# Optimization experiments

Hardware: AMD Instinct MI355X
Metric: run time of the kernel (lower is better)

## Reference

```python
import jax, jax.numpy as jnp
import numpy as np

EPS = 1e-5
DECAY = 0.9        # membrane potential decay
SLOPE = 0.01       # leaky_relu negative slope
HEBB_LR = 0.01     # Hebbian plasticity learning rate
WD = 1e-3          # synapse weight decay
W_CLAMP = 1.0      # synapse weight clamp


def _ln(x, g, b):
    mu = jnp.mean(x, axis=-1, keepdims=True)
    var = jnp.mean((x - mu) ** 2, axis=-1, keepdims=True)
    return (x - mu) * jax.lax.rsqrt(var + EPS) * g + b


def setup_inputs() -> dict:
    key = jax.random.key(0)
    ks = jax.random.split(key, 4)
    B, N = 16384, 1024
    scale = 1.0 / np.sqrt(N)
    return {
        "inputs": jax.random.normal(ks[0], (B, N), dtype=jnp.float32),
        "contribution": jax.random.uniform(ks[1], (B,), dtype=jnp.float32),
        "prev_potential": jnp.zeros((B, N), dtype=jnp.float32),
        "syn_weights": jax.random.normal(ks[2], (N, N), dtype=jnp.float32) * scale,
        "gate_W": jax.random.normal(ks[3], (N, N), dtype=jnp.float32) * scale,
        "gate_b": jnp.zeros((N,), dtype=jnp.float32),
        "pre_gamma": jnp.ones((N,), dtype=jnp.float32),
        "pre_beta": jnp.zeros((N,), dtype=jnp.float32),
        "ln_gamma": jnp.ones((N,), dtype=jnp.float32),
        "ln_beta": jnp.zeros((N,), dtype=jnp.float32),
    }


def reference(inputs, contribution, prev_potential, syn_weights, gate_W, gate_b,
              pre_gamma, pre_beta, ln_gamma, ln_beta):
    B = inputs.shape[0]
    # pre-norm
    x_norm = _ln(inputs, pre_gamma, pre_beta)
    # neuron: recurrent drive through synapse weights + leaky membrane
    pre = x_norm @ syn_weights                      # [B, N]
    potential = DECAY * prev_potential + pre        # new neuron state
    activation = jnp.where(potential >= 0, potential, SLOPE * potential)
    # Hebbian synapse update modulated by per-sample contribution
    hebb = jnp.einsum('bi,bj->ij', activation * contribution[:, None], activation) / B
    new_syn_weights = jnp.clip(syn_weights * (1.0 - WD) + HEBB_LR * hebb,
                               -W_CLAMP, W_CLAMP)
    # gated residual (gate computed on raw inputs)
    gate = jax.nn.sigmoid(inputs @ gate_W.T + gate_b)
    residual = gate * activation + (1.0 - gate) * inputs
    # post-norm (dropout is identity in eval/reference)
    output = _ln(residual, ln_gamma, ln_beta)
    return (output, potential, new_syn_weights)
```

## Files before the change

### kernel.cpp

```cpp
#include <hip/hip_runtime.h>
#include <cstdint>
#include <cstddef>

#define EPS 1e-5f
#define DECAY 0.9f
#define SLOPE 0.01f
#define HEBB_LR 0.01f
#define WDK 1e-3f

typedef float f32x4 __attribute__((ext_vector_type(4)));
typedef __bf16 bf16x8 __attribute__((ext_vector_type(8)));
typedef unsigned short u16;
typedef unsigned int u32;

union U128 { uint4 u; bf16x8 b; };
union Pack16 { u16 s[16]; uint4 q[2]; };
union Pack8  { u16 s[8];  uint4 q; };
union Pack4  { u16 s[4];  uint2 q; };

__device__ __forceinline__ u16 f2b(float f) {
  u32 u = __builtin_bit_cast(u32, f);
  u = u + 0x7FFFu + ((u >> 16) & 1u);
  return (u16)(u >> 16);
}
__device__ __forceinline__ float b2f(u16 h) {
  u32 u = ((u32)h) << 16;
  return __builtin_bit_cast(float, u);
}
__device__ __forceinline__ float wred(float x) {
#pragma unroll
  for (int o = 32; o > 0; o >>= 1) x += __shfl_down(x, o, 64);
  return x;
}

__device__ __forceinline__ void gld16(const u16* g, u16* lds) {
  __builtin_amdgcn_global_load_lds(
      (__attribute__((address_space(1))) void*)g,
      (__attribute__((address_space(3))) void*)lds, 16, 0, 0);
}

__global__ __launch_bounds__(256) void prep_rows(
    const float* __restrict__ in, const float* __restrict__ pg,
    const float* __restrict__ pb, u16* __restrict__ xnb,
    u16* __restrict__ inb, int N) {
  const int row = blockIdx.x, t = threadIdx.x;
  const float* rp = in + (size_t)row * N;
  float4 v = reinterpret_cast<const float4*>(rp)[t];
  float s = v.x + v.y + v.z + v.w;
  float s2 = v.x * v.x + v.y * v.y + v.z * v.z + v.w * v.w;
  s = wred(s); s2 = wred(s2);
  __shared__ float rs_[4], rs2_[4];
  if ((t & 63) == 0) { rs_[t >> 6] = s; rs2_[t >> 6] = s2; }
  __syncthreads();
  float S = rs_[0] + rs_[1] + rs_[2] + rs_[3];
  float S2 = rs2_[0] + rs2_[1] + rs2_[2] + rs2_[3];
  float mu = S / N;
  float var = S2 / N - mu * mu;
  float rstd = rsqrtf(var + EPS);
  float4 g = reinterpret_cast<const float4*>(pg)[t];
  float4 b = reinterpret_cast<const float4*>(pb)[t];
  float xv[4] = {v.x, v.y, v.z, v.w};
  float gv[4] = {g.x, g.y, g.z, g.w};
  float bv[4] = {b.x, b.y, b.z, b.w};
  Pack4 px, pi;
#pragma unroll
  for (int j = 0; j < 4; ++j) {
    px.s[j] = f2b((xv[j] - mu) * rstd * gv[j] + bv[j]);
    pi.s[j] = f2b(xv[j]);
  }
  reinterpret_cast<uint2*>(xnb + (size_t)row * N)[t] = px.q;
  reinterpret_cast<uint2*>(inb + (size_t)row * N)[t] = pi.q;
}

__global__ __launch_bounds__(256) void wconv(const float* __restrict__ W,
                                             u16* __restrict__ Wb, int total) {
  int idx = blockIdx.x * 256 + threadIdx.x;
  size_t off = (size_t)idx * 8;
  if (off >= (size_t)total) return;
  float4 a = *reinterpret_cast<const float4*>(W + off);
  float4 b = *reinterpret_cast<const float4*>(W + off + 4);
  Pack8 p;
  p.s[0] = f2b(a.x); p.s[1] = f2b(a.y); p.s[2] = f2b(a.z); p.s[3] = f2b(a.w);
  p.s[4] = f2b(b.x); p.s[5] = f2b(b.y); p.s[6] = f2b(b.z); p.s[7] = f2b(b.w);
  *reinterpret_cast<uint4*>(Wb + off) = p.q;
}

__global__ __launch_bounds__(256) void wconv_T(const float* __restrict__ W,
                                               u16* __restrict__ Wt, int R, int C) {
  __shared__ float tile[64][65];
  int c0 = blockIdx.x * 64, r0 = blockIdx.y * 64;
  int tr = threadIdx.x >> 2, tc = threadIdx.x & 3;
#pragma unroll
  for (int cc = 0; cc < 4; ++cc) {
    float4 v = *reinterpret_cast<const float4*>(W + (size_t)(r0 + tr) * C + c0 + tc * 16 + cc * 4);
    tile[tr][tc * 16 + cc * 4 + 0] = v.x;
    tile[tr][tc * 16 + cc * 4 + 1] = v.y;
    tile[tr][tc * 16 + cc * 4 + 2] = v.z;
    tile[tr][tc * 16 + cc * 4 + 3] = v.w;
  }
  __syncthreads();
  Pack16 p;
#pragma unroll
  for (int j = 0; j < 16; ++j) p.s[j] = f2b(tile[tc * 16 + j][tr]);
  uint4* dst = reinterpret_cast<uint4*>(Wt + (size_t)(c0 + tr) * R + r0 + tc * 16);
  dst[0] = p.q[0]; dst[1] = p.q[1];
}

__global__ __launch_bounds__(256) void transpose_act(
    const float* __restrict__ pot, const float* __restrict__ contrib,
    u16* __restrict__ actT, u16* __restrict__ actcT, int Brows, int N) {
  __shared__ float tile[64][65];
  __shared__ float csh[64];
  int n0 = blockIdx.x * 64, b0 = blockIdx.y * 64;
  int tr = threadIdx.x >> 2, tc = threadIdx.x & 3;
  if (threadIdx.x < 64) csh[threadIdx.x] = contrib[b0 + threadIdx.x];
#pragma unroll
  for (int cc = 0; cc < 4; ++cc) {
    float4 v = *reinterpret_cast<const float4*>(pot + (size_t)(b0 + tr) * N + n0 + tc * 16 + cc * 4);
    float a0 = v.x >= 0.f ? v.x : SLOPE * v.x;
    float a1 = v.y >= 0.f ? v.y : SLOPE * v.y;
    float a2 = v.z >= 0.f ? v.z : SLOPE * v.z;
    float a3 = v.w >= 0.f ? v.w : SLOPE * v.w;
    tile[tr][tc * 16 + cc * 4 + 0] = a0;
    tile[tr][tc * 16 + cc * 4 + 1] = a1;
    tile[tr][tc * 16 + cc * 4 + 2] = a2;
    tile[tr][tc * 16 + cc * 4 + 3] = a3;
  }
  __syncthreads();
  Pack16 pa, pc;
#pragma unroll
  for (int j = 0; j < 16; ++j) {
    float a = tile[tc * 16 + j][tr];
    pa.s[j] = f2b(a);
    pc.s[j] = f2b(a * csh[tc * 16 + j]);
  }
  size_t obase = (size_t)(n0 + tr) * Brows + b0 + tc * 16;
  uint4* d1 = reinterpret_cast<uint4*>(actT + obase);
  d1[0] = pa.q[0]; d1[1] = pa.q[1];
  uint4* d2 = reinterpret_cast<uint4*>(actcT + obase);
  d2[0] = pc.q[0]; d2[1] = pc.q[1];
}

__global__ __launch_bounds__(256) void fuse_out(
    const float* __restrict__ pot, const u16* __restrict__ gate,
    const float* __restrict__ in, const float* __restrict__ lg,
    const float* __restrict__ lb, float* __restrict__ out, int N) {
  const int row = blockIdx.x, t = threadIdx.x;
  size_t base = (size_t)row * N;
  float4 p = reinterpret_cast<const float4*>(pot + base)[t];
  float4 x = reinterpret_cast<const float4*>(in + base)[t];
  Pack4 gq; gq.q = reinterpret_cast<const uint2*>(gate + base)[t];
  float pv[4] = {p.x, p.y, p.z, p.w}, xv[4] = {x.x, x.y, x.z, x.w};
  float res[4];
  float s = 0.f, s2 = 0.f;
#pragma unroll
  for (int j = 0; j < 4; ++j) {
    float a = pv[j] >= 0.f ? pv[j] : SLOPE * pv[j];
    float gv = b2f(gq.s[j]);
    float r = gv * a + (1.f - gv) * xv[j];
    res[j] = r; s += r; s2 += r * r;
  }
  s = wred(s); s2 = wred(s2);
  __shared__ float rs_[4], rs2_[4];
  if ((t & 63) == 0) { rs_[t >> 6] = s; rs2_[t >> 6] = s2; }
  __syncthreads();
  float S = rs_[0] + rs_[1] + rs_[2] + rs_[3];
  float S2 = rs2_[0] + rs2_[1] + rs2_[2] + rs2_[3];
  float mu = S / N, var = S2 / N - mu * mu, rstd = rsqrtf(var + EPS);
  float4 g4 = reinterpret_cast<const float4*>(lg)[t];
  float4 b4 = reinterpret_cast<const float4*>(lb)[t];
  float gv[4] = {g4.x, g4.y, g4.z, g4.w}, bv[4] = {b4.x, b4.y, b4.z, b4.w};
  float4 o;
  o.x = (res[0] - mu) * rstd * gv[0] + bv[0];
  o.y = (res[1] - mu) * rstd * gv[1] + bv[1];
  o.z = (res[2] - mu) * rstd * gv[2] + bv[2];
  o.w = (res[3] - mu) * rstd * gv[3] + bv[3];
  reinterpret_cast<float4*>(out + base)[t] = o;
}

__device__ __forceinline__ u32 swz64(u32 b) { return b ^ (((b >> 7) & 3u) << 4); }

__device__ __forceinline__ void stage8(int s, int NT4, const u16* A, const u16* Bt,
                                       int m0, int n0, int lda, int kbase,
                                       char* ldsc, int tid) {
  if (s >= NT4) return;
  const int tau = s >> 2, j = s & 3;
  const int mat = j & 1, ks = j >> 1;
  const u16* src = mat ? Bt : A;
  const int rbase = mat ? n0 : m0;
  const int kk = kbase + tau * 64 + ks * 32;
  char* dst = ldsc + (tau & 1) * 65536 + mat * 32768 + ks * 16384 + tid * 16;
  const int row = tid >> 2;
  const int kg = (tid & 3) ^ ((tid >> 3) & 3);
  const u16* g0 = src + (size_t)(rbase + row) * (size_t)lda + kk + kg * 8;
  gld16(g0, (u16*)dst);
  gld16(g0 + (size_t)128 * (size_t)lda, (u16*)(dst + 8192));
}

#define VMW(n) asm volatile("s_waitcnt vmcnt(" #n ")" ::: "memory")
#define BARR() asm volatile("s_barrier" ::: "memory")

template <int EPI>
__global__ __launch_bounds__(512, 2) void gemm8p(
    const u16* __restrict__ A, const u16* __restrict__ Bt,
    int lda, int NT, int Ncols,
    const float* __restrict__ aux,
    float* __restrict__ outF, u16* __restrict__ outB,
    int nbx, int nbxShift, int nbyX) {
  __shared__ __align__(128) u16 lds[65536];
  char* ldsc = (char*)lds;
  const int tid = threadIdx.x;
  const int w = tid >> 6, l = tid & 63;
  const int wr = w >> 2, wc = w & 3;
  const int r16 = l & 15, gq = l >> 4;

  int bx, by, kb;
  if (EPI == 2) {
    bx = blockIdx.x; by = blockIdx.y; kb = blockIdx.z * NT * 64;
  } else {
    int bid = blockIdx.x;
    int xcd = bid & 7, i = bid >> 3;
    by = xcd * nbyX + (i >> nbxShift);
    bx = i & (nbx - 1);
    kb = 0;
  }
  const int m0 = by * 256, n0 = bx * 256;
  const int NT4 = NT * 4;

  int pA[8], pB[4];
#pragma unroll
  for (int mf = 0; mf < 8; ++mf)
    pA[mf] = (int)swz64((u32)((wr * 128 + mf * 16 + r16) * 64 + gq * 16));
#pragma unroll
  for (int nf = 0; nf < 4; ++nf)
    pB[nf] = (int)swz64((u32)((wc * 64 + nf * 16 + r16) * 64 + gq * 16));

  f32x4 acc[8][4] = {};
  U128 af[8], bf[2];

#define LDA_(ks) { char* _b = ldsc + buf * 65536 + (ks) * 16384;              \
  _Pragma("unroll") for (int mf = 0; mf < 8; ++mf)                            \
    af[mf].u = *reinterpret_cast<const uint4*>(_b + pA[mf]); }
#define LDB_(ks, nh) { char* _b = ldsc + buf * 65536 + 32768 + (ks) * 16384;  \
  bf[0].u = *reinterpret_cast<const uint4*>(_b + pB[2 * (nh)]);               \
  bf[1].u = *reinterpret_cast<const uint4*>(_b + pB[2 * (nh) + 1]); }
#define MFMA_(nh) { __builtin_amdgcn_s_setprio(1);                            \
  _Pragma("unroll") for (int mf = 0; mf < 8; ++mf) {                          \
    acc[mf][2 * (nh)] = __builtin_amdgcn_mfma_f32_16x16x32_bf16(              \
        af[mf].b, bf[0].b, acc[mf][2 * (nh)], 0, 0, 0);                       \
    acc[mf][2 * (nh) + 1] = __builtin_amdgcn_mfma_f32_16x16x32_bf16(          \
        af[mf].b, bf[1].b, acc[mf][2 * (nh) + 1], 0, 0, 0); }                 \
  __builtin_amdgcn_s_setprio(0); }
#define STG(s) stage8((s), NT4, A, Bt, m0, n0, lda, kb, ldsc, tid)

  for (int s = 0; s < 6; ++s) STG(s);
  VMW(8); BARR();

  for (int t = 0; t < NT - 1; ++t) {
    const int buf = t & 1;
    const int sb = t * 4;
    LDA_(0); LDB_(0, 0); STG(sb + 6); VMW(8); BARR(); MFMA_(0); BARR();
    LDB_(0, 1);          STG(sb + 7); VMW(8); BARR(); MFMA_(1); BARR();
    LDA_(1); LDB_(1, 0); STG(sb + 8); VMW(8); BARR(); MFMA_(0); BARR();
    LDB_(1, 1);          STG(sb + 9);
    if (t == NT - 2) { VMW(4); } else { VMW(8); }
    BARR(); MFMA_(1); BARR();
  }
  {
    const int buf = (NT - 1) & 1;
    LDA_(0); LDB_(0, 0); MFMA_(0);
    LDB_(0, 1);          MFMA_(1);
    VMW(0); BARR();
    LDA_(1); LDB_(1, 0); MFMA_(0);
    LDB_(1, 1);          MFMA_(1);
  }
#undef LDA_
#undef LDB_
#undef MFMA_
#undef STG

  const size_t splitOff =
      (EPI == 2) ? (size_t)blockIdx.z * (size_t)Ncols * (size_t)(gridDim.y * 256) : 0;
#pragma unroll
  for (int mf = 0; mf < 8; ++mf) {
#pragma unroll
    for (int r = 0; r < 4; ++r) {
      const int m = m0 + wr * 128 + mf * 16 + gq * 4 + r;
#pragma unroll
      for (int nf = 0; nf < 4; ++nf) {
        const int n = n0 + wc * 64 + nf * 16 + r16;
        float v = acc[mf][nf][r];
        if (EPI == 0) {
          size_t off = (size_t)m * Ncols + n;
          outF[off] = DECAY * aux[off] + v;
        } else if (EPI == 1) {
          float gl = v + aux[n];
          outB[(size_t)m * Ncols + n] = f2b(1.f / (1.f + __expf(-gl)));
        } else {
          outB[splitOff + (size_t)m * Ncols + n] = f2b(v);
        }
      }
    }
  }
}

__global__ __launch_bounds__(256) void syn_update(
    const float* __restrict__ syn, const u16* __restrict__ part,
    float* __restrict__ outS, int total8, float hebbScale, int nsplit, int NN) {
  int idx = blockIdx.x * 256 + threadIdx.x;
  if (idx >= total8) return;
  float h[8] = {0.f, 0.f, 0.f, 0.f, 0.f, 0.f, 0.f, 0.f};
  for (int sp = 0; sp < nsplit; ++sp) {
    Pack8 p;
    p.q = reinterpret_cast<const uint4*>(part + (size_t)sp * NN)[idx];
#pragma unroll
    for (int j = 0; j < 8; ++j) h[j] += b2f(p.s[j]);
  }
  float4 s0 = reinterpret_cast<const float4*>(syn)[idx * 2];
  float4 s1 = reinterpret_cast<const float4*>(syn)[idx * 2 + 1];
  float sv[8] = {s0.x, s0.y, s0.z, s0.w, s1.x, s1.y, s1.z, s1.w};
  float ov[8];
#pragma unroll
  for (int j = 0; j < 8; ++j)
    ov[j] = fminf(1.f, fmaxf(-1.f, sv[j] * (1.f - WDK) + hebbScale * h[j]));
  float4 o0 = {ov[0], ov[1], ov[2], ov[3]};
  float4 o1 = {ov[4], ov[5], ov[6], ov[7]};
  reinterpret_cast<float4*>(outS)[idx * 2] = o0;
  reinterpret_cast<float4*>(outS)[idx * 2 + 1] = o1;
}

extern "C" void kernel_launch(void* const* d_in, const int* in_sizes, int n_in,
                              void* d_out, int out_size, void* d_ws, size_t ws_size,
                              hipStream_t stream) {
  const float* inputs        = (const float*)d_in[0];
  const float* contribution  = (const float*)d_in[1];
  const float* prev_potential= (const float*)d_in[2];
  const float* syn_weights   = (const float*)d_in[3];
  const float* gate_W        = (const float*)d_in[4];
  const float* gate_b        = (const float*)d_in[5];
  const float* pre_gamma     = (const float*)d_in[6];
  const float* pre_beta      = (const float*)d_in[7];
  const float* ln_gamma      = (const float*)d_in[8];
  const float* ln_beta       = (const float*)d_in[9];

  const int B = in_sizes[1];
  const int N = in_sizes[5];
  const size_t BN = (size_t)B * N;

  float* out_output = (float*)d_out;
  float* out_pot    = out_output + BN;
  float* out_syn    = out_output + 2 * BN;

  char* ws = (char*)d_ws;
  u16* xnb   = (u16*)ws;
  u16* inb   = (u16*)(ws + BN * 2);
  u16* synT  = (u16*)(ws + BN * 4);
  u16* gwb   = (u16*)(ws + BN * 4 + (size_t)N * N * 2);
  u16* gateb = (u16*)(ws + BN * 4 + (size_t)N * N * 4);
  u16* actT  = xnb;
  u16* actcT = inb;
  u16* part  = gateb;

  const int NS = 16;
  const int NT = N / 64;

  prep_rows<<<B, 256, 0, stream>>>(inputs, pre_gamma, pre_beta, xnb, inb, N);
  wconv_T<<<dim3(N / 64, N / 64), 256, 0, stream>>>(syn_weights, synT, N, N);
  wconv<<<(N * N / 8 + 255) / 256, 256, 0, stream>>>(gate_W, gwb, N * N);

  const int nbx = N / 256, nbxShift = 2, nbyX = (B / 256) / 8;
  gemm8p<0><<<(B / 256) * (N / 256), 512, 0, stream>>>(
      xnb, synT, N, NT, N, prev_potential, out_pot, nullptr, nbx, nbxShift, nbyX);
  gemm8p<1><<<(B / 256) * (N / 256), 512, 0, stream>>>(
      inb, gwb, N, NT, N, gate_b, nullptr, gateb, nbx, nbxShift, nbyX);
  fuse_out<<<B, 256, 0, stream>>>(out_pot, gateb, inputs, ln_gamma, ln_beta, out_output, N);
  transpose_act<<<dim3(N / 64, B / 64), 256, 0, stream>>>(
      out_pot, contribution, actT, actcT, B, N);
  gemm8p<2><<<dim3(N / 256, N / 256, NS), 512, 0, stream>>>(
      actcT, actT, B, (B / NS) / 64, N, nullptr, nullptr, part, 0, 0, 0);
  syn_update<<<(N * N / 8 + 255) / 256, 256, 0, stream>>>(
      syn_weights, part, out_syn, N * N / 8, HEBB_LR / (float)B, NS, N * N);
}
```

Before: 445.0 us.

## Replace fine-grained 8-phase GEMM pipeline with simpler double-buffered k-loop

Replaces the GEMM mainloop's interleaved quarter-tile staging and per-phase vmcnt waits and barriers with a plain double-buffered loop. Each iteration stages a full 64-wide K slice into the other 64KB buffer, then runs all 32 MFMAs per k-step, using a new XOR swizzle over 128-byte rows. LDS grows to 128KB per block, which probably breaks the requested 2-blocks-per-CU occupancy, and there is only one barrier per tile. Separately, fuse_out now reads the bf16 copy of the inputs instead of fp32, which cuts traffic but lowers the precision of the residual term.

Measured after the change: 438.0 us. Within noise of the previous version (-1.6%).

```diff
diff --git a/kernel.cpp b/kernel.cpp
--- a/kernel.cpp
+++ b/kernel.cpp
@@ -143,21 +143,22 @@
 
 __global__ __launch_bounds__(256) void fuse_out(
     const float* __restrict__ pot, const u16* __restrict__ gate,
-    const float* __restrict__ in, const float* __restrict__ lg,
+    const u16* __restrict__ inb, const float* __restrict__ lg,
     const float* __restrict__ lb, float* __restrict__ out, int N) {
   const int row = blockIdx.x, t = threadIdx.x;
   size_t base = (size_t)row * N;
   float4 p = reinterpret_cast<const float4*>(pot + base)[t];
-  float4 x = reinterpret_cast<const float4*>(in + base)[t];
+  Pack4 xq; xq.q = reinterpret_cast<const uint2*>(inb + base)[t];
   Pack4 gq; gq.q = reinterpret_cast<const uint2*>(gate + base)[t];
-  float pv[4] = {p.x, p.y, p.z, p.w}, xv[4] = {x.x, x.y, x.z, x.w};
+  float pv[4] = {p.x, p.y, p.z, p.w};
   float res[4];
   float s = 0.f, s2 = 0.f;
 #pragma unroll
   for (int j = 0; j < 4; ++j) {
     float a = pv[j] >= 0.f ? pv[j] : SLOPE * pv[j];
     float gv = b2f(gq.s[j]);
-    float r = gv * a + (1.f - gv) * xv[j];
+    float xv = b2f(xq.s[j]);
+    float r = gv * a + (1.f - gv) * xv;
     res[j] = r; s += r; s2 += r * r;
   }
   s = wred(s); s2 = wred(s2);
@@ -178,37 +179,14 @@
   reinterpret_cast<float4*>(out + base)[t] = o;
 }
 
-__device__ __forceinline__ u32 swz64(u32 b) { return b ^ (((b >> 7) & 3u) << 4); }
-
-__device__ __forceinline__ void stage8(int s, int NT4, const u16* A, const u16* Bt,
-                                       int m0, int n0, int lda, int kbase,
-                                       char* ldsc, int tid) {
-  if (s >= NT4) return;
-  const int tau = s >> 2, j = s & 3;
-  const int mat = j & 1, ks = j >> 1;
-  const u16* src = mat ? Bt : A;
-  const int rbase = mat ? n0 : m0;
-  const int kk = kbase + tau * 64 + ks * 32;
-  char* dst = ldsc + (tau & 1) * 65536 + mat * 32768 + ks * 16384 + tid * 16;
-  const int row = tid >> 2;
-  const int kg = (tid & 3) ^ ((tid >> 3) & 3);
-  const u16* g0 = src + (size_t)(rbase + row) * (size_t)lda + kk + kg * 8;
-  gld16(g0, (u16*)dst);
-  gld16(g0 + (size_t)128 * (size_t)lda, (u16*)(dst + 8192));
-}
-
-#define VMW(n) asm volatile("s_waitcnt vmcnt(" #n ")" ::: "memory")
-#define BARR() asm volatile("s_barrier" ::: "memory")
-
 template <int EPI>
-__global__ __launch_bounds__(512, 2) void gemm8p(
+__global__ __launch_bounds__(512, 2) void gemm2p(
     const u16* __restrict__ A, const u16* __restrict__ Bt,
     int lda, int NT, int Ncols,
     const float* __restrict__ aux,
     float* __restrict__ outF, u16* __restrict__ outB,
     int nbx, int nbxShift, int nbyX) {
-  __shared__ __align__(128) u16 lds[65536];
-  char* ldsc = (char*)lds;
+  __shared__ __align__(128) char lds[131072];
   const int tid = threadIdx.x;
   const int w = tid >> 6, l = tid & 63;
   const int wr = w >> 2, wc = w & 3;
@@ -225,59 +203,64 @@
     kb = 0;
   }
   const int m0 = by * 256, n0 = bx * 256;
-  const int NT4 = NT * 4;
-
-  int pA[8], pB[4];
-#pragma unroll
-  for (int mf = 0; mf < 8; ++mf)
-    pA[mf] = (int)swz64((u32)((wr * 128 + mf * 16 + r16) * 64 + gq * 16));
-#pragma unroll
-  for (int nf = 0; nf < 4; ++nf)
-    pB[nf] = (int)swz64((u32)((wc * 64 + nf * 16 + r16) * 64 + gq * 16));
+
+  const u16* gA[4]; const u16* gB[4]; int dOff[4];
+#pragma unroll
+  for (int i = 0; i < 4; ++i) {
+    int c = i * 512 + tid;
+    int row = c >> 3;
+    int kg = (c & 7) ^ (row & 7);
+    gA[i] = A + (size_t)(m0 + row) * (size_t)lda + kb + kg * 8;
+    gB[i] = Bt + (size_t)(n0 + row) * (size_t)lda + kb + kg * 8;
+    dOff[i] = c * 16;
+  }
+
+  int pA[8], pB[4], kgx[2];
+#pragma unroll
+  for (int mf = 0; mf < 8; ++mf) pA[mf] = (wr * 128 + mf * 16 + r16) * 128;
+#pragma unroll
+  for (int nf = 0; nf < 4; ++nf) pB[nf] = (wc * 64 + nf * 16 + r16) * 128;
+  kgx[0] = ((gq) ^ (r16 & 7)) * 16;
+  kgx[1] = ((4 + gq) ^ (r16 & 7)) * 16;
 
   f32x4 acc[8][4] = {};
-  U128 af[8], bf[2];
-
-#define LDA_(ks) { char* _b = ldsc + buf * 65536 + (ks) * 16384;              \
-  _Pragma("unroll") for (int mf = 0; mf < 8; ++mf)                            \
-    af[mf].u = *reinterpret_cast<const uint4*>(_b + pA[mf]); }
-#define LDB_(ks, nh) { char* _b = ldsc + buf * 65536 + 32768 + (ks) * 16384;  \
-  bf[0].u = *reinterpret_cast<const uint4*>(_b + pB[2 * (nh)]);               \
-  bf[1].u = *reinterpret_cast<const uint4*>(_b + pB[2 * (nh) + 1]); }
-#define MFMA_(nh) { __builtin_amdgcn_s_setprio(1);                            \
-  _Pragma("unroll") for (int mf = 0; mf < 8; ++mf) {                          \
-    acc[mf][2 * (nh)] = __builtin_amdgcn_mfma_f32_16x16x32_bf16(              \
-        af[mf].b, bf[0].b, acc[mf][2 * (nh)], 0, 0, 0);                       \
-    acc[mf][2 * (nh) + 1] = __builtin_amdgcn_mfma_f32_16x16x32_bf16(          \
-        af[mf].b, bf[1].b, acc[mf][2 * (nh) + 1], 0, 0, 0); }                 \
-  __builtin_amdgcn_s_setprio(0); }
-#define STG(s) stage8((s), NT4, A, Bt, m0, n0, lda, kb, ldsc, tid)
-
-  for (int s = 0; s < 6; ++s) STG(s);
-  VMW(8); BARR();
-
-  for (int t = 0; t < NT - 1; ++t) {
-    const int buf = t & 1;
-    const int sb = t * 4;
-    LDA_(0); LDB_(0, 0); STG(sb + 6); VMW(8); BARR(); MFMA_(0); BARR();
-    LDB_(0, 1);          STG(sb + 7); VMW(8); BARR(); MFMA_(1); BARR();
-    LDA_(1); LDB_(1, 0); STG(sb + 8); VMW(8); BARR(); MFMA_(0); BARR();
-    LDB_(1, 1);          STG(sb + 9);
-    if (t == NT - 2) { VMW(4); } else { VMW(8); }
-    BARR(); MFMA_(1); BARR();
-  }
-  {
-    const int buf = (NT - 1) & 1;
-    LDA_(0); LDB_(0, 0); MFMA_(0);
-    LDB_(0, 1);          MFMA_(1);
-    VMW(0); BARR();
-    LDA_(1); LDB_(1, 0); MFMA_(0);
-    LDB_(1, 1);          MFMA_(1);
-  }
-#undef LDA_
-#undef LDB_
-#undef MFMA_
-#undef STG
+
+#define STAGE_(t, bufb) { const int _kk = (t) * 64;                           \
+  _Pragma("unroll") for (int i = 0; i < 4; ++i)                               \
+    gld16(gA[i] + _kk, (u16*)(lds + (bufb) + dOff[i]));                       \
+  _Pragma("unroll") for (int i = 0; i < 4; ++i)                               \
+    gld16(gB[i] + _kk, (u16*)(lds + (bufb) + 32768 + dOff[i])); }
+
+  STAGE_(0, 0);
+  __syncthreads();
+
+  int buf = 0;
+  for (int t = 0; t < NT; ++t) {
+    if (t + 1 < NT) STAGE_(t + 1, (buf ^ 1) * 65536);
+    const char* Ab = lds + buf * 65536;
+    const char* Bb = Ab + 32768;
+#pragma unroll
+    for (int ks = 0; ks < 2; ++ks) {
+      U128 af[8], bf[4];
+#pragma unroll
+      for (int mf = 0; mf < 8; ++mf)
+        af[mf].u = *reinterpret_cast<const uint4*>(Ab + pA[mf] + kgx[ks]);
+#pragma unroll
+      for (int nf = 0; nf < 4; ++nf)
+        bf[nf].u = *reinterpret_cast<const uint4*>(Bb + pB[nf] + kgx[ks]);
+      __builtin_amdgcn_s_setprio(1);
+#pragma unroll
+      for (int mf = 0; mf < 8; ++mf)
+#pragma unroll
+        for (int nf = 0; nf < 4; ++nf)
+          acc[mf][nf] = __builtin_amdgcn_mfma_f32_16x16x32_bf16(
+              af[mf].b, bf[nf].b, acc[mf][nf], 0, 0, 0);
+      __builtin_amdgcn_s_setprio(0);
+    }
+    __syncthreads();
+    buf ^= 1;
+  }
+#undef STAGE_
 
   const size_t splitOff =
       (EPI == 2) ? (size_t)blockIdx.z * (size_t)Ncols * (size_t)(gridDim.y * 256) : 0;
@@ -369,14 +352,14 @@
   wconv<<<(N * N / 8 + 255) / 256, 256, 0, stream>>>(gate_W, gwb, N * N);
 
   const int nbx = N / 256, nbxShift = 2, nbyX = (B / 256) / 8;
-  gemm8p<0><<<(B / 256) * (N / 256), 512, 0, stream>>>(
+  gemm2p<0><<<(B / 256) * (N / 256), 512, 0, stream>>>(
       xnb, synT, N, NT, N, prev_potential, out_pot, nullptr, nbx, nbxShift, nbyX);
-  gemm8p<1><<<(B / 256) * (N / 256), 512, 0, stream>>>(
+  gemm2p<1><<<(B / 256) * (N / 256), 512, 0, stream>>>(
       inb, gwb, N, NT, N, gate_b, nullptr, gateb, nbx, nbxShift, nbyX);
-  fuse_out<<<B, 256, 0, stream>>>(out_pot, gateb, inputs, ln_gamma, ln_beta, out_output, N);
+  fuse_out<<<B, 256, 0, stream>>>(out_pot, gateb, inb, ln_gamma, ln_beta, out_output, N);
   transpose_act<<<dim3(N / 64, B / 64), 256, 0, stream>>>(
       out_pot, contribution, actT, actcT, B, N);
-  gemm8p<2><<<dim3(N / 256, N / 256, NS), 512, 0, stream>>>(
+  gemm2p<2><<<dim3(N / 256, N / 256, NS), 512, 0, stream>>>(
       actcT, actT, B, (B / NS) / 64, N, nullptr, nullptr, part, 0, 0, 0);
   syn_update<<<(N * N / 8 + 255) / 256, 256, 0, stream>>>(
       syn_weights, part, out_syn, N * N / 8, HEBB_LR / (float)B, NS, N * N);
```
